# Kernel optimization log

Measured on AMD Instinct MI355X. Metric: run time of the kernel, lower is better.

## Reference

```python
import jax, jax.numpy as jnp
import numpy as np

K = 2          # superpatch hop size (init kwarg)
BN_EPS = 1e-5  # torch BatchNorm2d default eps


def setup_inputs() -> dict:
    key = jax.random.key(0)
    ks = jax.random.split(key, 7)
    B, C, H, W = 32, 192, 56, 56
    Co = 2 * C  # out_channels must equal 2*in_channels for the BN to type-check
    x = jax.random.normal(ks[0], (B, C, H, W), jnp.float32)
    # 1x1 conv: weight [Co, 2C] (kernel dims squeezed), bias [Co]
    W_conv = jax.random.normal(ks[1], (Co, 2 * C), jnp.float32) * (1.0 / np.sqrt(2 * C))
    b_conv = jax.random.normal(ks[2], (Co,), jnp.float32) * 0.02
    # BatchNorm2d(2C) affine params + running stats (inference mode)
    gamma = 1.0 + 0.1 * jax.random.normal(ks[3], (Co,), jnp.float32)
    beta = 0.1 * jax.random.normal(ks[4], (Co,), jnp.float32)
    run_mean = 0.1 * jax.random.normal(ks[5], (Co,), jnp.float32)
    run_var = jax.random.uniform(ks[6], (Co,), jnp.float32, 0.5, 1.5)
    return {"x": x, "W_conv": W_conv, "b_conv": b_conv, "gamma": gamma,
            "beta": beta, "run_mean": run_mean, "run_var": run_var}


def _max_relative(x0, axis, n_steps):
    """Accumulate max(0, x0 - roll(x0, -i*K, axis)) for i=1..n_steps via scan.
    Carry keeps the running rolled tensor so each step rolls by only -K."""
    def step(carry, _):
        xr, xj = carry
        xr = jnp.roll(xr, -K, axis=axis)
        xj = jnp.maximum(xj, x0 - xr)
        return (xr, xj), None
    (_, xj), _ = jax.lax.scan(step, (x0, jnp.zeros_like(x0)), None, length=n_steps)
    return xj


def reference(x, W_conv, b_conv, gamma, beta, run_mean, run_var):
    B, C, H, W = x.shape
    # center the superpatch: roll by -(K//2) in both spatial dims
    x0 = jnp.roll(x, (-(K // 2), -(K // 2)), axis=(2, 3))
    # max-relative aggregation over row shifts then column shifts
    # torch.arange(K, H, K) has (H-1)//K elements
    xj_h = _max_relative(x0, axis=2, n_steps=(H - 1) // K)
    xj_w = _max_relative(x0, axis=3, n_steps=(W - 1) // K)
    xj = jnp.maximum(xj_h, xj_w)  # both loops fold into the same running max (init 0)
    xc = jnp.concatenate([x0, xj], axis=1)              # [B, 2C, H, W]
    xc = jnp.roll(xc, (K // 2, K // 2), axis=(2, 3))    # undo the centering roll
    # 1x1 conv == per-pixel GEMM
    y = jnp.einsum('bchw,oc->bohw', xc, W_conv) + b_conv[None, :, None, None]
    # BatchNorm2d in inference mode (running stats)
    scale = gamma * jax.lax.rsqrt(run_var + BN_EPS)
    y = y * scale[None, :, None, None] + (beta - run_mean * scale)[None, :, None, None]
    return jax.nn.gelu(y, approximate=False)  # torch nn.GELU default = exact erf
```

## Files before the change

kernel.cpp:

```cpp
#include <hip/hip_runtime.h>
#include <cstdint>

#define B_N 32
#define C_N 192
#define W_N 56
#define HW_N 3136
#define CO_N 384
#define K_N 384
#define M_N 100352

typedef unsigned short u16;
typedef unsigned int u32;
typedef __attribute__((ext_vector_type(8))) short short8;
typedef __attribute__((ext_vector_type(4))) float floatx4;

__device__ __forceinline__ u16 bf16rne(float f) {
  union { float f; u32 u; } v; v.f = f;
  u32 r = (v.u + 0x7FFFu + ((v.u >> 16) & 1u)) >> 16;
  return (u16)r;
}

__device__ __forceinline__ void stage16(const void* g, void* lbase, int lane) {
#if __has_builtin(__builtin_amdgcn_global_load_lds)
  __builtin_amdgcn_global_load_lds(
      (const __attribute__((address_space(1))) void*)(uintptr_t)g,
      (__attribute__((address_space(3))) void*)(u32)(uintptr_t)lbase,
      16, 0, 0);
#else
  *(uint4*)((char*)lbase + lane * 16) = *(const uint4*)g;
#endif
}

__global__ __launch_bounds__(256) void prep_consts(
    const float* __restrict__ Wc, const float* __restrict__ bconv,
    const float* __restrict__ gamma, const float* __restrict__ beta,
    const float* __restrict__ rmean, const float* __restrict__ rvar,
    u16* __restrict__ Wbf, float* __restrict__ alphaV, float* __restrict__ betaV) {
  int idx = blockIdx.x * 256 + threadIdx.x;
  if (idx < CO_N * K_N) Wbf[idx] = bf16rne(Wc[idx]);
  if (idx < CO_N) {
    float s = gamma[idx] * rsqrtf(rvar[idx] + 1e-5f);
    alphaV[idx] = s;
    betaV[idx] = bconv[idx] * s + beta[idx] - rmean[idx] * s;
  }
}

#define PLN_F 3192
#define WSLOT 3640

__global__ __launch_bounds__(128) void xj_compute(const float* __restrict__ x,
                                                  u16* __restrict__ XJ) {
  __shared__ float sm[2 * WSLOT];
  int tid = threadIdx.x;
  int wid = tid >> 6, lane = tid & 63;
  float* pl  = sm + wid * WSLOT;
  float* rs1 = pl + PLN_F;
  float* rs2 = rs1 + 112;
  float* cs1 = rs2 + 112;
  float* cs2 = cs1 + 112;
  size_t base = ((size_t)blockIdx.x * 2 + wid) * HW_N;
  const float4* xg4 = (const float4*)(x + base);

  #pragma unroll 1
  for (int i = lane; i < 784; i += 64) {
    float4 v = xg4[i];
    int h = i / 14;
    int w0 = (i - h * 14) * 4;
    float* d = pl + h * 57 + w0;
    d[0] = v.x; d[1] = v.y; d[2] = v.z; d[3] = v.w;
  }
  asm volatile("s_waitcnt lgkmcnt(0)" ::: "memory");
  __builtin_amdgcn_wave_barrier();

  if (lane < 56) {
    float r1a = 3e38f, r2a = 3e38f, r1b = 3e38f, r2b = 3e38f;
    float c1a = 3e38f, c2a = 3e38f, c1b = 3e38f, c2b = 3e38f;
    const float* rowp = pl + lane * 57;
    #pragma unroll
    for (int i = 0; i < 28; ++i) {
      float va = pl[(2 * i) * 57 + lane];
      float vb = pl[(2 * i + 1) * 57 + lane];
      float wa = rowp[2 * i];
      float wb = rowp[2 * i + 1];
      r2a = fminf(r2a, fmaxf(r1a, va)); r1a = fminf(r1a, va);
      r2b = fminf(r2b, fmaxf(r1b, vb)); r1b = fminf(r1b, vb);
      c2a = fminf(c2a, fmaxf(c1a, wa)); c1a = fminf(c1a, wa);
      c2b = fminf(c2b, fmaxf(c1b, wb)); c1b = fminf(c1b, wb);
    }
    rs1[lane] = r1a; rs1[56 + lane] = r1b;
    rs2[lane] = r2a; rs2[56 + lane] = r2b;
    cs1[lane] = c1a; cs1[56 + lane] = c1b;
    cs2[lane] = c2a; cs2[56 + lane] = c2b;
  }
  asm volatile("s_waitcnt lgkmcnt(0)" ::: "memory");
  __builtin_amdgcn_wave_barrier();

  u16* op = XJ + base;
  #pragma unroll 1
  for (int i = lane; i < 784; i += 64) {
    int idx = i * 4;
    int h = i / 14;
    int w0 = (i - h * 14) * 4;
    int hp = h & 1;
    const float* pr = pl + h * 57 + w0;
    float4 s1 = *(const float4*)(rs1 + hp * 56 + w0);
    float4 s2 = *(const float4*)(rs2 + hp * 56 + w0);
    float c1e = cs1[h], c1o = cs1[56 + h];
    float c2e = cs2[h], c2o = cs2[56 + h];
    ushort4 o;
    u16* opx = &o.x;
    const float* s1p = &s1.x; const float* s2p = &s2.x;
    #pragma unroll
    for (int j = 0; j < 4; ++j) {
      int wv = w0 + j;
      float v = pr[j];
      float rm = (v == s1p[j]) ? s2p[j] : s1p[j];
      float cm;
      if ((wv & 1) == 0) cm = (v == c1e) ? c2e : c1e;
      else               cm = (v == c1o) ? c2o : c1o;
      float xj = v - fminf(rm, cm);
      opx[j] = bf16rne(fmaxf(xj, 0.0f));
    }
    *(ushort4*)(op + idx) = o;
  }
}


__device__ __forceinline__ void load_pk(int s, u32 pk[2][4],
                                        const float* __restrict__ x,
                                        const u16* __restrict__ XJ,
                                        const u32* offs, int kp) {
  if (s < 3) {
    int c0 = s * 64;
    #pragma unroll
    for (int r = 0; r < 2; ++r) {
      const float* a = x + (size_t)offs[r] + (size_t)(c0 + 2 * kp) * HW_N;
      float4 v0 = *(const float4*)a;
      float4 v1 = *(const float4*)(a + HW_N);
      const float* f0 = &v0.x; const float* f1 = &v1.x;
      #pragma unroll
      for (int j = 0; j < 4; ++j)
        pk[r][j] = (u32)bf16rne(f0[j]) | ((u32)bf16rne(f1[j]) << 16);
    }
  } else {
    int c0 = (s - 3) * 64;
    #pragma unroll
    for (int r = 0; r < 2; ++r) {
      const u16* a = XJ + (size_t)offs[r] + (size_t)(c0 + 2 * kp) * HW_N;
      ushort4 v0 = *(const ushort4*)a;
      ushort4 v1 = *(const ushort4*)(a + HW_N);
      const u16* q0 = &v0.x; const u16* q1 = &v1.x;
      #pragma unroll
      for (int j = 0; j < 4; ++j)
        pk[r][j] = (u32)q0[j] | ((u32)q1[j] << 16);
    }
  }
}

__global__ __launch_bounds__(512) void gemm_fused(
    const float* __restrict__ x, const u16* __restrict__ XJ,
    const u16* __restrict__ Wbf,
    const float* __restrict__ alphaV, const float* __restrict__ betaV,
    float* __restrict__ out) {
  __shared__ __align__(16) char smem_raw[65536];
  u16* As = (u16*)smem_raw;
  u32* As32 = (u32*)smem_raw;
  u16* Bs = (u16*)(smem_raw + 16384);
  float* ep = (float*)smem_raw;
  int tid = threadIdx.x;
  int lane = tid & 63;
  int w = tid >> 6;
  int wm = w & 1, wn = w >> 1;
  int l15 = lane & 15, quad = lane >> 4;
  int m0 = blockIdx.x << 7;

  int kp = tid >> 4;
  int pxq = tid & 15;
  u32 offs[2];
  #pragma unroll
  for (int r = 0; r < 2; ++r) {
    int gm = m0 + (pxq + 16 * r) * 4;
    int bb = gm / HW_N;
    int pp = gm - bb * HW_N;
    offs[r] = (u32)bb * (u32)(C_N * HW_N) + (u32)pp;
  }
  int lrow = lane >> 3;
  int lchunk = lane & 7;

  floatx4 acc[4][6];
  #pragma unroll
  for (int i = 0; i < 4; ++i)
    #pragma unroll
    for (int j = 0; j < 6; ++j) acc[i][j] = (floatx4)0.0f;

  u32 pk[2][4];
  load_pk(0, pk, x, XJ, offs, kp);

  #pragma unroll 1
  for (int ko = 0; ko < 6; ++ko) {
    int c0 = (ko < 3 ? ko * 64 : (ko - 3) * 64);
    int kbase = (ko < 3 ? 0 : 192);
    __syncthreads();
    #pragma unroll
    for (int c = 0; c < 6; ++c) {
      int rowbase = w * 48 + c * 8;
      int row = rowbase + lrow;
      int chunk = lchunk ^ (row & 7);
      stage16(Wbf + (size_t)row * K_N + kbase + c0 + chunk * 8,
              Bs + rowbase * 64, lane);
    }
    #pragma unroll
    for (int r = 0; r < 2; ++r) {
      #pragma unroll
      for (int j = 0; j < 4; ++j) {
        int px = (pxq + 16 * r) * 4 + j;
        As32[px * 32 + (kp & 3) + (((kp >> 2) ^ ((px >> 1) & 7)) << 2)] = pk[r][j];
      }
    }
    __syncthreads();
    u32 pkn[2][4];
    if (ko < 5) load_pk(ko + 1, pkn, x, XJ, offs, kp);
    #pragma unroll
    for (int h2 = 0; h2 < 2; ++h2) {
      short8 aF[4], bF[6];
      #pragma unroll
      for (int mi = 0; mi < 4; ++mi) {
        int r = wm * 64 + mi * 16 + l15;
        aF[mi] = *(const short8*)(As + r * 64 + (((h2 * 4 + quad) ^ ((r >> 1) & 7)) << 3));
      }
      #pragma unroll
      for (int ni = 0; ni < 6; ++ni) {
        int r = wn * 96 + ni * 16 + l15;
        bF[ni] = *(const short8*)(Bs + r * 64 + (((h2 * 4 + quad) ^ (r & 7)) << 3));
      }
      #pragma unroll
      for (int mi = 0; mi < 4; ++mi)
        #pragma unroll
        for (int ni = 0; ni < 6; ++ni)
          acc[mi][ni] = __builtin_amdgcn_mfma_f32_16x16x32_bf16(
              aF[mi], bF[ni], acc[mi][ni], 0, 0, 0);
    }
    if (ko < 5) {
      #pragma unroll
      for (int r = 0; r < 2; ++r)
        #pragma unroll
        for (int j = 0; j < 4; ++j) pk[r][j] = pkn[r][j];
    }
  }

  float av[6], bv[6];
  #pragma unroll
  for (int ni = 0; ni < 6; ++ni) {
    int o = wn * 96 + ni * 16 + l15;
    av[ni] = alphaV[o];
    bv[ni] = betaV[o];
  }
  #pragma unroll 1
  for (int oc = 0; oc < 4; ++oc) {
    __syncthreads();
    if (wn == oc) {
      #pragma unroll
      for (int ni = 0; ni < 6; ++ni) {
        #pragma unroll
        for (int mi = 0; mi < 4; ++mi) {
          floatx4 a = acc[mi][ni];
          float4 g;
          float* gp = &g.x;
          #pragma unroll
          for (int i = 0; i < 4; ++i) {
            float t = a[i] * av[ni] + bv[ni];
            gp[i] = 0.5f * t * (1.0f + erff(t * 0.70710678118654752f));
          }
          *(float4*)&ep[(ni * 16 + l15) * 132 + wm * 64 + mi * 16 + quad * 4] = g;
        }
      }
    }
    __syncthreads();
    #pragma unroll
    for (int it = 0; it < 6; ++it) {
      int task = tid + it * 512;
      int r = task >> 5;
      int c4 = task & 31;
      float4 v = *(float4*)&ep[r * 132 + c4 * 4];
      int gm = m0 + c4 * 4;
      int bb = gm / HW_N;
      int pp = gm - bb * HW_N;
      *(float4*)(out + ((size_t)(bb * CO_N + oc * 96 + r)) * HW_N + pp) = v;
    }
  }
}

extern "C" void kernel_launch(void* const* d_in, const int* in_sizes, int n_in,
                              void* d_out, int out_size, void* d_ws, size_t ws_size,
                              hipStream_t stream) {
  const float* x  = (const float*)d_in[0];
  const float* Wc = (const float*)d_in[1];
  const float* bc = (const float*)d_in[2];
  const float* gm = (const float*)d_in[3];
  const float* bt = (const float*)d_in[4];
  const float* rm = (const float*)d_in[5];
  const float* rv = (const float*)d_in[6];
  float* out = (float*)d_out;

  char* ws = (char*)d_ws;
  size_t offXJ = 0;
  size_t offWb = offXJ + (size_t)B_N * C_N * HW_N * 2;
  size_t offAl = offWb + (size_t)CO_N * K_N * 2;
  u16* XJ = (u16*)(ws + offXJ);
  u16* Wbf = (u16*)(ws + offWb);
  float* alphaV = (float*)(ws + offAl);
  float* betaV = alphaV + CO_N;

  hipLaunchKernelGGL(prep_consts, dim3(576), dim3(256), 0, stream,
                     Wc, bc, gm, bt, rm, rv, Wbf, alphaV, betaV);
  hipLaunchKernelGGL(xj_compute, dim3(B_N * C_N / 2), dim3(128), 0, stream, x, XJ);
  hipLaunchKernelGGL(gemm_fused, dim3(M_N / 128), dim3(512), 0, stream,
                     x, XJ, Wbf, alphaV, betaV, out);
}
```

Measured before the change: 349.6 us.

## Compute max-relative features inside GEMM from per-plane min statistics

Instead of writing a full bf16 XJ tensor and reading it back in the GEMM, a smaller pre-pass now stores only per-channel row/column min and second-min statistics. The GEMM's operand loader rebuilds the xj values on the fly from x and those statistics. The weight columns are permuted so each K-tile interleaves x and xj channels, letting each thread pack both into one LDS store. This removes a full-size intermediate write and read, at the cost of extra ALU work and extra small statistic loads inside the GEMM main loop.

```diff
diff --git a/kernel.cpp b/kernel.cpp
--- a/kernel.cpp
+++ b/kernel.cpp
@@ -8,10 +8,12 @@
 #define CO_N 384
 #define K_N 384
 #define M_N 100352
+#define ST_F 448
 
 typedef unsigned short u16;
 typedef unsigned int u32;
 typedef __attribute__((ext_vector_type(8))) short short8;
+typedef __attribute__((ext_vector_type(2))) unsigned int u32x2;
 typedef __attribute__((ext_vector_type(4))) float floatx4;
 
 __device__ __forceinline__ u16 bf16rne(float f) {
@@ -37,7 +39,13 @@
     const float* __restrict__ rmean, const float* __restrict__ rvar,
     u16* __restrict__ Wbf, float* __restrict__ alphaV, float* __restrict__ betaV) {
   int idx = blockIdx.x * 256 + threadIdx.x;
-  if (idx < CO_N * K_N) Wbf[idx] = bf16rne(Wc[idx]);
+  if (idx < CO_N * K_N) {
+    int o = idx / K_N, K = idx - o * K_N;
+    int ko = K >> 6, t = K & 63;
+    int ch = 32 * ko + 2 * (t >> 2) + (t & 1);
+    int src = ch + ((t & 2) ? 192 : 0);
+    Wbf[idx] = bf16rne(Wc[o * K_N + src]);
+  }
   if (idx < CO_N) {
     float s = gamma[idx] * rsqrtf(rvar[idx] + 1e-5f);
     alphaV[idx] = s;
@@ -46,119 +54,53 @@
 }
 
 #define PLN_F 3192
-#define WSLOT 3640
-
-__global__ __launch_bounds__(128) void xj_compute(const float* __restrict__ x,
-                                                  u16* __restrict__ XJ) {
-  __shared__ float sm[2 * WSLOT];
+
+__global__ __launch_bounds__(128) void struct_compute(const float* __restrict__ x,
+                                                      float* __restrict__ ST) {
+  __shared__ float pl[PLN_F];
   int tid = threadIdx.x;
-  int wid = tid >> 6, lane = tid & 63;
-  float* pl  = sm + wid * WSLOT;
-  float* rs1 = pl + PLN_F;
-  float* rs2 = rs1 + 112;
-  float* cs1 = rs2 + 112;
-  float* cs2 = cs1 + 112;
-  size_t base = ((size_t)blockIdx.x * 2 + wid) * HW_N;
-  const float4* xg4 = (const float4*)(x + base);
-
+  size_t pbase = (size_t)blockIdx.x * HW_N;
+  const float4* xg4 = (const float4*)(x + pbase);
   #pragma unroll 1
-  for (int i = lane; i < 784; i += 64) {
+  for (int i = tid; i < 784; i += 128) {
     float4 v = xg4[i];
     int h = i / 14;
     int w0 = (i - h * 14) * 4;
     float* d = pl + h * 57 + w0;
     d[0] = v.x; d[1] = v.y; d[2] = v.z; d[3] = v.w;
   }
-  asm volatile("s_waitcnt lgkmcnt(0)" ::: "memory");
-  __builtin_amdgcn_wave_barrier();
-
-  if (lane < 56) {
+  __syncthreads();
+  float* st = ST + (size_t)blockIdx.x * ST_F;
+  if (tid < 56) {
     float r1a = 3e38f, r2a = 3e38f, r1b = 3e38f, r2b = 3e38f;
+    #pragma unroll
+    for (int i = 0; i < 28; ++i) {
+      float va = pl[(2 * i) * 57 + tid];
+      float vb = pl[(2 * i + 1) * 57 + tid];
+      r2a = fminf(r2a, fmaxf(r1a, va)); r1a = fminf(r1a, va);
+      r2b = fminf(r2b, fmaxf(r1b, vb)); r1b = fminf(r1b, vb);
+    }
+    st[tid] = r1a;       st[56 + tid] = r1b;
+    st[112 + tid] = r2a; st[168 + tid] = r2b;
+  } else if (tid >= 64 && tid < 120) {
+    int h = tid - 64;
+    const float* rowp = pl + h * 57;
     float c1a = 3e38f, c2a = 3e38f, c1b = 3e38f, c2b = 3e38f;
-    const float* rowp = pl + lane * 57;
     #pragma unroll
     for (int i = 0; i < 28; ++i) {
-      float va = pl[(2 * i) * 57 + lane];
-      float vb = pl[(2 * i + 1) * 57 + lane];
       float wa = rowp[2 * i];
       float wb = rowp[2 * i + 1];
-      r2a = fminf(r2a, fmaxf(r1a, va)); r1a = fminf(r1a, va);
-      r2b = fminf(r2b, fmaxf(r1b, vb)); r1b = fminf(r1b, vb);
       c2a = fminf(c2a, fmaxf(c1a, wa)); c1a = fminf(c1a, wa);
       c2b = fminf(c2b, fmaxf(c1b, wb)); c1b = fminf(c1b, wb);
     }
-    rs1[lane] = r1a; rs1[56 + lane] = r1b;
-    rs2[lane] = r2a; rs2[56 + lane] = r2b;
-    cs1[lane] = c1a; cs1[56 + lane] = c1b;
-    cs2[lane] = c2a; cs2[56 + lane] = c2b;
-  }
-  asm volatile("s_waitcnt lgkmcnt(0)" ::: "memory");
-  __builtin_amdgcn_wave_barrier();
-
-  u16* op = XJ + base;
-  #pragma unroll 1
-  for (int i = lane; i < 784; i += 64) {
-    int idx = i * 4;
-    int h = i / 14;
-    int w0 = (i - h * 14) * 4;
-    int hp = h & 1;
-    const float* pr = pl + h * 57 + w0;
-    float4 s1 = *(const float4*)(rs1 + hp * 56 + w0);
-    float4 s2 = *(const float4*)(rs2 + hp * 56 + w0);
-    float c1e = cs1[h], c1o = cs1[56 + h];
-    float c2e = cs2[h], c2o = cs2[56 + h];
-    ushort4 o;
-    u16* opx = &o.x;
-    const float* s1p = &s1.x; const float* s2p = &s2.x;
-    #pragma unroll
-    for (int j = 0; j < 4; ++j) {
-      int wv = w0 + j;
-      float v = pr[j];
-      float rm = (v == s1p[j]) ? s2p[j] : s1p[j];
-      float cm;
-      if ((wv & 1) == 0) cm = (v == c1e) ? c2e : c1e;
-      else               cm = (v == c1o) ? c2o : c1o;
-      float xj = v - fminf(rm, cm);
-      opx[j] = bf16rne(fmaxf(xj, 0.0f));
-    }
-    *(ushort4*)(op + idx) = o;
-  }
-}
-
-
-__device__ __forceinline__ void load_pk(int s, u32 pk[2][4],
-                                        const float* __restrict__ x,
-                                        const u16* __restrict__ XJ,
-                                        const u32* offs, int kp) {
-  if (s < 3) {
-    int c0 = s * 64;
-    #pragma unroll
-    for (int r = 0; r < 2; ++r) {
-      const float* a = x + (size_t)offs[r] + (size_t)(c0 + 2 * kp) * HW_N;
-      float4 v0 = *(const float4*)a;
-      float4 v1 = *(const float4*)(a + HW_N);
-      const float* f0 = &v0.x; const float* f1 = &v1.x;
-      #pragma unroll
-      for (int j = 0; j < 4; ++j)
-        pk[r][j] = (u32)bf16rne(f0[j]) | ((u32)bf16rne(f1[j]) << 16);
-    }
-  } else {
-    int c0 = (s - 3) * 64;
-    #pragma unroll
-    for (int r = 0; r < 2; ++r) {
-      const u16* a = XJ + (size_t)offs[r] + (size_t)(c0 + 2 * kp) * HW_N;
-      ushort4 v0 = *(const ushort4*)a;
-      ushort4 v1 = *(const ushort4*)(a + HW_N);
-      const u16* q0 = &v0.x; const u16* q1 = &v1.x;
-      #pragma unroll
-      for (int j = 0; j < 4; ++j)
-        pk[r][j] = (u32)q0[j] | ((u32)q1[j] << 16);
-    }
-  }
-}
+    st[224 + 2 * h] = c1a; st[225 + 2 * h] = c1b;
+    st[336 + 2 * h] = c2a; st[337 + 2 * h] = c2b;
+  }
+}
+
 
 __global__ __launch_bounds__(512) void gemm_fused(
-    const float* __restrict__ x, const u16* __restrict__ XJ,
+    const float* __restrict__ x, const float* __restrict__ ST,
     const u16* __restrict__ Wbf,
     const float* __restrict__ alphaV, const float* __restrict__ betaV,
     float* __restrict__ out) {
@@ -174,16 +116,19 @@
   int l15 = lane & 15, quad = lane >> 4;
   int m0 = blockIdx.x << 7;
 
-  int kp = tid >> 4;
-  int pxq = tid & 15;
-  u32 offs[2];
-  #pragma unroll
-  for (int r = 0; r < 2; ++r) {
-    int gm = m0 + (pxq + 16 * r) * 4;
-    int bb = gm / HW_N;
-    int pp = gm - bb * HW_N;
-    offs[r] = (u32)bb * (u32)(C_N * HW_N) + (u32)pp;
-  }
+  int cp = tid >> 5;
+  int pxq = tid & 31;
+  int gm = m0 + pxq * 4;
+  int bb = gm / HW_N;
+  int pp = gm - bb * HW_N;
+  int hh = pp / W_N;
+  int w0 = pp - hh * W_N;
+  int hp = hh & 1;
+  const float* xbase = x + (size_t)bb * (C_N * HW_N) + pp;
+  const float* stbase = ST + (size_t)bb * (C_N * ST_F);
+  int hpw = hp * 56 + w0;
+  int csoff = 224 + 2 * hh;
+
   int lrow = lane >> 3;
   int lchunk = lane & 7;
 
@@ -193,33 +138,68 @@
     #pragma unroll
     for (int j = 0; j < 6; ++j) acc[i][j] = (floatx4)0.0f;
 
-  u32 pk[2][4];
-  load_pk(0, pk, x, XJ, offs, kp);
+  u32 pkx[4], pkj[4];
+  auto load_pk = [&](int s, u32* ox, u32* oj) {
+    int ch0 = 32 * s + 2 * cp;
+    const float* xa = xbase + (size_t)ch0 * HW_N;
+    float4 v0 = *(const float4*)xa;
+    float4 v1 = *(const float4*)(xa + HW_N);
+    const float* sb0 = stbase + (size_t)ch0 * ST_F;
+    const float* sb1 = sb0 + ST_F;
+    float4 r10 = *(const float4*)(sb0 + hpw);
+    float4 r20 = *(const float4*)(sb0 + 112 + hpw);
+    float2 c10 = *(const float2*)(sb0 + csoff);
+    float2 c20 = *(const float2*)(sb0 + csoff + 112);
+    float4 r11 = *(const float4*)(sb1 + hpw);
+    float4 r21 = *(const float4*)(sb1 + 112 + hpw);
+    float2 c11 = *(const float2*)(sb1 + csoff);
+    float2 c21 = *(const float2*)(sb1 + csoff + 112);
+    const float* f0 = &v0.x; const float* f1 = &v1.x;
+    const float* r10p = &r10.x; const float* r20p = &r20.x;
+    const float* r11p = &r11.x; const float* r21p = &r21.x;
+    #pragma unroll
+    for (int j = 0; j < 4; ++j) {
+      float a = f0[j], b = f1[j];
+      ox[j] = (u32)bf16rne(a) | ((u32)bf16rne(b) << 16);
+      float rm0 = (a == r10p[j]) ? r20p[j] : r10p[j];
+      float rm1 = (b == r11p[j]) ? r21p[j] : r11p[j];
+      float cm0, cm1;
+      if ((j & 1) == 0) {
+        cm0 = (a == c10.x) ? c20.x : c10.x;
+        cm1 = (b == c11.x) ? c21.x : c11.x;
+      } else {
+        cm0 = (a == c10.y) ? c20.y : c10.y;
+        cm1 = (b == c11.y) ? c21.y : c11.y;
+      }
+      float xj0 = fmaxf(a - fminf(rm0, cm0), 0.0f);
+      float xj1 = fmaxf(b - fminf(rm1, cm1), 0.0f);
+      oj[j] = (u32)bf16rne(xj0) | ((u32)bf16rne(xj1) << 16);
+    }
+  };
+
+  load_pk(0, pkx, pkj);
 
   #pragma unroll 1
   for (int ko = 0; ko < 6; ++ko) {
-    int c0 = (ko < 3 ? ko * 64 : (ko - 3) * 64);
-    int kbase = (ko < 3 ? 0 : 192);
     __syncthreads();
     #pragma unroll
     for (int c = 0; c < 6; ++c) {
       int rowbase = w * 48 + c * 8;
       int row = rowbase + lrow;
       int chunk = lchunk ^ (row & 7);
-      stage16(Wbf + (size_t)row * K_N + kbase + c0 + chunk * 8,
+      stage16(Wbf + (size_t)row * K_N + ko * 64 + chunk * 8,
               Bs + rowbase * 64, lane);
     }
     #pragma unroll
-    for (int r = 0; r < 2; ++r) {
-      #pragma unroll
-      for (int j = 0; j < 4; ++j) {
-        int px = (pxq + 16 * r) * 4 + j;
-        As32[px * 32 + (kp & 3) + (((kp >> 2) ^ ((px >> 1) & 7)) << 2)] = pk[r][j];
-      }
-    }
-    __syncthreads();
-    u32 pkn[2][4];
-    if (ko < 5) load_pk(ko + 1, pkn, x, XJ, offs, kp);
+    for (int j = 0; j < 4; ++j) {
+      int px = pxq * 4 + j;
+      int chunk = (cp >> 1) ^ ((px >> 1) & 7);
+      u32x2 d; d.x = pkx[j]; d.y = pkj[j];
+      *(u32x2*)(As32 + px * 32 + chunk * 4 + 2 * (cp & 1)) = d;
+    }
+    __syncthreads();
+    u32 pnx[4], pnj[4];
+    if (ko < 5) load_pk(ko + 1, pnx, pnj);
     #pragma unroll
     for (int h2 = 0; h2 < 2; ++h2) {
       short8 aF[4], bF[6];
@@ -242,9 +222,7 @@
     }
     if (ko < 5) {
       #pragma unroll
-      for (int r = 0; r < 2; ++r)
-        #pragma unroll
-        for (int j = 0; j < 4; ++j) pk[r][j] = pkn[r][j];
+      for (int j = 0; j < 4; ++j) { pkx[j] = pnx[j]; pkj[j] = pnj[j]; }
     }
   }
 
@@ -282,10 +260,10 @@
       int r = task >> 5;
       int c4 = task & 31;
       float4 v = *(float4*)&ep[r * 132 + c4 * 4];
-      int gm = m0 + c4 * 4;
-      int bb = gm / HW_N;
-      int pp = gm - bb * HW_N;
-      *(float4*)(out + ((size_t)(bb * CO_N + oc * 96 + r)) * HW_N + pp) = v;
+      int g = m0 + c4 * 4;
+      int b2 = g / HW_N;
+      int p2 = g - b2 * HW_N;
+      *(float4*)(out + ((size_t)(b2 * CO_N + oc * 96 + r)) * HW_N + p2) = v;
     }
   }
 }
@@ -303,17 +281,17 @@
   float* out = (float*)d_out;
 
   char* ws = (char*)d_ws;
-  size_t offXJ = 0;
-  size_t offWb = offXJ + (size_t)B_N * C_N * HW_N * 2;
+  size_t offST = 0;
+  size_t offWb = offST + (size_t)B_N * C_N * ST_F * 4;
   size_t offAl = offWb + (size_t)CO_N * K_N * 2;
-  u16* XJ = (u16*)(ws + offXJ);
+  float* ST = (float*)(ws + offST);
   u16* Wbf = (u16*)(ws + offWb);
   float* alphaV = (float*)(ws + offAl);
   float* betaV = alphaV + CO_N;
 
   hipLaunchKernelGGL(prep_consts, dim3(576), dim3(256), 0, stream,
                      Wc, bc, gm, bt, rm, rv, Wbf, alphaV, betaV);
-  hipLaunchKernelGGL(xj_compute, dim3(B_N * C_N / 2), dim3(128), 0, stream, x, XJ);
+  hipLaunchKernelGGL(struct_compute, dim3(B_N * C_N), dim3(128), 0, stream, x, ST);
   hipLaunchKernelGGL(gemm_fused, dim3(M_N / 128), dim3(512), 0, stream,
-                     x, XJ, Wbf, alphaV, betaV, out);
-}
+                     x, ST, Wbf, alphaV, betaV, out);
+}
```

New measurement: 332.8 us. -4.8%, faster.
